# Kernel optimization log

Measured on AMD Instinct MI355X. Metric: run time of the kernel, lower is better.

## Reference

```python
import jax, jax.numpy as jnp
import numpy as np

D_MODEL = 768
NUM_HEADS = 12
D_K = D_MODEL // NUM_HEADS


def setup_inputs() -> dict:
    key = jax.random.key(0)
    ks = jax.random.split(key, 12)
    B, S = 4, 2048
    s = 1.0 / np.sqrt(D_MODEL)
    inp = {
        "query": jax.random.normal(ks[0], (B, S, D_MODEL), jnp.float32),
        "key": jax.random.normal(ks[1], (B, S, D_MODEL), jnp.float32),
        "value": jax.random.normal(ks[2], (B, S, D_MODEL), jnp.float32),
        "Wq": jax.random.normal(ks[3], (D_MODEL, D_MODEL), jnp.float32) * s,
        "bq": jnp.zeros((D_MODEL,), jnp.float32),
        "Wk": jax.random.normal(ks[4], (D_MODEL, D_MODEL), jnp.float32) * s,
        "bk": jnp.zeros((D_MODEL,), jnp.float32),
        "Wv": jax.random.normal(ks[5], (D_MODEL, D_MODEL), jnp.float32) * s,
        "bv": jnp.zeros((D_MODEL,), jnp.float32),
        "Wo": jax.random.normal(ks[6], (D_MODEL, D_MODEL), jnp.float32) * s,
        "bo": jnp.zeros((D_MODEL,), jnp.float32),
    }
    return inp


def _split_heads(x):
    B, S, _ = x.shape
    return x.reshape(B, S, NUM_HEADS, D_K).transpose(0, 2, 1, 3)  # [B,H,S,Dk]


def reference(query, key, value, Wq, bq, Wk, bk, Wv, bv, Wo, bo):
    # Linear projections (torch nn.Linear: x @ W.T + b)
    Q = _split_heads(query @ Wq.T + bq)
    K = _split_heads(key @ Wk.T + bk)
    V = _split_heads(value @ Wv.T + bv)
    scale = 1.0 / jnp.sqrt(jnp.asarray(D_K, Q.dtype))
    scores = jnp.einsum("bhqd,bhkd->bhqk", Q, K) * scale  # [B,H,S,S]
    attn = jax.nn.softmax(scores, axis=-1)
    # dropout is identity in eval mode
    out = jnp.einsum("bhqk,bhkd->bhqd", attn, V)  # [B,H,S,Dk]
    B, H, S, Dk = out.shape
    out = out.transpose(0, 2, 1, 3).reshape(B, S, H * Dk)
    return out @ Wo.T + bo
```

## Files before the change

### kernel.cpp

```cpp
#include <hip/hip_runtime.h>
#include <hip/hip_bf16.h>

typedef _Float16 half8 __attribute__((ext_vector_type(8)));
typedef _Float16 h4 __attribute__((ext_vector_type(4)));
typedef __fp16 fp16x2 __attribute__((ext_vector_type(2)));
typedef float f32x4 __attribute__((ext_vector_type(4)));

#define D_MODEL 768
#define NUM_HEADS 12
#define D_K 64
#define SEQ 2048
#define BATCH 4
#define M_TOTAL (BATCH * SEQ)
#define W_ELEMS (D_MODEL * D_MODEL)
#define X_ELEMS (M_TOTAL * D_MODEL)
#define QSCALE 0.18033688011112042f
#define SOFF 4.0f

__device__ __forceinline__ void gll16(const _Float16* g, _Float16* l) {
    __builtin_amdgcn_global_load_lds(
        (const __attribute__((address_space(1))) unsigned int*)g,
        (__attribute__((address_space(3))) unsigned int*)l,
        16, 0, 0);
}

__device__ __forceinline__ void pk2(float a, float b, _Float16* out) {
    fp16x2 r = __builtin_amdgcn_cvt_pkrtz(a, b);
    out[0] = (_Float16)r[0];
    out[1] = (_Float16)r[1];
}

__global__ void convert_all(
    const float* __restrict__ w0, const float* __restrict__ w1,
    const float* __restrict__ w2, const float* __restrict__ w3,
    const float* __restrict__ x0, const float* __restrict__ x1,
    const float* __restrict__ x2, _Float16* __restrict__ dst)
{
    const size_t W4 = W_ELEMS / 4, X4 = X_ELEMS / 4;
    size_t i = (size_t)blockIdx.x * blockDim.x + threadIdx.x;
    const float* src;
    size_t off;
    if (i < 4 * W4) {
        size_t slab = i / W4;
        off = i - slab * W4;
        src = (slab == 0) ? w0 : (slab == 1) ? w1 : (slab == 2) ? w2 : w3;
    } else {
        size_t j = i - 4 * W4;
        size_t slab = j / X4;
        off = j - slab * X4;
        src = (slab == 0) ? x0 : (slab == 1) ? x1 : x2;
    }
    float4 f = ((const float4*)src)[off];
    h4 h;
    h[0] = (_Float16)f.x; h[1] = (_Float16)f.y;
    h[2] = (_Float16)f.z; h[3] = (_Float16)f.w;
    ((h4*)dst)[i] = h;
}

__global__ __launch_bounds__(256) void gemm_qkv(
    const _Float16* __restrict__ Xall, const _Float16* __restrict__ Wall,
    const float* __restrict__ bq, const float* __restrict__ bk, const float* __restrict__ bv,
    _Float16* __restrict__ Qo, _Float16* __restrict__ Ko, _Float16* __restrict__ Vto)
{
    __shared__ __align__(16) char smem[36864];
    _Float16* As = (_Float16*)smem;
    _Float16* Bs = As + 128 * 64;

    const int z = blockIdx.z;
    const _Float16* X = Xall + (size_t)z * X_ELEMS;
    const _Float16* W = Wall + (size_t)z * W_ELEMS;

    const int t = threadIdx.x;
    const int w = t >> 6;
    const int l = t & 63;
    const int ln = t & 15;
    const int quad = (t >> 4) & 3;
    const int wm = w >> 1, wn = w & 1;
    const int m0 = blockIdx.x * 128, n0 = blockIdx.y * 128;

    const int srow = l >> 3;
    const int scol = (l & 7) ^ srow;

    f32x4 acc[4][4] = {};

    for (int k0 = 0; k0 < D_MODEL; k0 += 64) {
#pragma unroll
        for (int jj = 0; jj < 4; ++jj) {
            int j = w * 4 + jj;
            int row = j * 8 + srow;
            gll16(X + (size_t)(m0 + row) * D_MODEL + k0 + scol * 8, As + j * 512);
            gll16(W + (size_t)(n0 + row) * D_MODEL + k0 + scol * 8, Bs + j * 512);
        }
        __syncthreads();

#pragma unroll
        for (int kk = 0; kk < 2; ++kk) {
            half8 a[4], b[4];
#pragma unroll
            for (int i = 0; i < 4; ++i) {
                int ra = wm * 64 + i * 16 + ln;
                int rb = wn * 64 + i * 16 + ln;
                a[i] = *(const half8*)&As[ra * 64 + (((kk * 4 + quad) ^ (ln & 7)) * 8)];
                b[i] = *(const half8*)&Bs[rb * 64 + (((kk * 4 + quad) ^ (ln & 7)) * 8)];
            }
#pragma unroll
            for (int i = 0; i < 4; ++i)
#pragma unroll
                for (int j2 = 0; j2 < 4; ++j2)
                    acc[i][j2] = __builtin_amdgcn_mfma_f32_16x16x32_f16(a[i], b[j2], acc[i][j2], 0, 0, 0);
        }
        __syncthreads();
    }

    const float* bias = (z == 0) ? bq : (z == 1) ? bk : bv;
    if (z <= 1) {
        _Float16* dst = (z == 0) ? Qo : Ko;
#pragma unroll
        for (int i = 0; i < 4; ++i) {
#pragma unroll
            for (int j = 0; j < 4; ++j) {
                int n = n0 + wn * 64 + j * 16 + ln;
                int h = n >> 6, d = n & 63;
                float bn = bias[n];
#pragma unroll
                for (int r = 0; r < 4; ++r) {
                    int m = m0 + wm * 64 + i * 16 + quad * 4 + r;
                    int b_ = m >> 11, s_ = m & 2047;
                    float v = acc[i][j][r] + bn;
                    if (z == 0) v *= QSCALE;
                    dst[((size_t)((b_ * NUM_HEADS + h) * SEQ + s_)) * D_K + d] = (_Float16)v;
                }
            }
        }
    } else {
        _Float16* T = (_Float16*)smem + (size_t)w * (64 * 72);
#pragma unroll
        for (int i = 0; i < 4; ++i) {
#pragma unroll
            for (int j = 0; j < 4; ++j) {
                float bn = bias[n0 + wn * 64 + j * 16 + ln];
                h4 hh;
#pragma unroll
                for (int r = 0; r < 4; ++r) hh[r] = (_Float16)(acc[i][j][r] + bn);
                *(h4*)&T[(j * 16 + ln) * 72 + i * 16 + quad * 4] = hh;
            }
        }
        const int b_ = m0 >> 11;
        const int s0 = (m0 & 2047) + wm * 64;
        const int head = (n0 >> 6) + wn;
        _Float16* base = Vto + (size_t)(b_ * NUM_HEADS + head) * D_K * SEQ + s0;
#pragma unroll
        for (int r8 = 0; r8 < 8; ++r8) {
            int nl = r8 * 8 + (l >> 3);
            half8 v = *(const half8*)&T[nl * 72 + (l & 7) * 8];
            *(half8*)(base + (size_t)nl * SEQ + (l & 7) * 8) = v;
        }
    }
}

__global__ __launch_bounds__(256) void attn(
    const _Float16* __restrict__ Qg, const _Float16* __restrict__ Kg,
    const _Float16* __restrict__ Vtg, _Float16* __restrict__ ctx)
{
    __shared__ __align__(16) _Float16 Ks[2][64 * 64];
    __shared__ __align__(16) _Float16 Vs[2][64 * 64];

    const int t = threadIdx.x;
    const int w = t >> 6;
    const int l = t & 63;
    const int ln = t & 15;
    const int quad = (t >> 4) & 3;
    const int bh = blockIdx.y;
    const int q0 = blockIdx.x * 128 + w * 32;

    const _Float16* Qh = Qg + (size_t)bh * SEQ * D_K;
    const _Float16* Kh = Kg + (size_t)bh * SEQ * D_K;
    const _Float16* Vh = Vtg + (size_t)bh * D_K * SEQ;

    const int srow = l >> 3;
    const int scol = (l & 7) ^ srow;
    const int j0 = w * 2, j1 = w * 2 + 1;
    const _Float16* Ksrc0 = Kh + (size_t)(j0 * 8 + srow) * D_K + scol * 8;
    const _Float16* Ksrc1 = Kh + (size_t)(j1 * 8 + srow) * D_K + scol * 8;
    const _Float16* Vsrc0 = Vh + (size_t)(j0 * 8 + srow) * SEQ + scol * 8;
    const _Float16* Vsrc1 = Vh + (size_t)(j1 * 8 + srow) * SEQ + scol * 8;

    half8 qf[2][2];
#pragma unroll
    for (int qt = 0; qt < 2; ++qt)
#pragma unroll
        for (int dh = 0; dh < 2; ++dh)
            qf[qt][dh] = *(const half8*)(Qh + (size_t)(q0 + qt * 16 + ln) * D_K + dh * 32 + quad * 8);

    f32x4 acc[2][4] = {};
    f32x4 lsum[2] = {};

    gll16(Ksrc0, &Ks[0][j0 * 512]);
    gll16(Ksrc1, &Ks[0][j1 * 512]);
    gll16(Vsrc0, &Vs[0][j0 * 512]);
    gll16(Vsrc1, &Vs[0][j1 * 512]);
    __syncthreads();

    for (int c = 0; c < SEQ / 64; ++c) {
        const int cur = c & 1;
        if (c + 1 < SEQ / 64) {
            const size_t koff = (size_t)(c + 1) * 64 * D_K;
            const size_t voff = (size_t)(c + 1) * 64;
            gll16(Ksrc0 + koff, &Ks[cur ^ 1][j0 * 512]);
            gll16(Ksrc1 + koff, &Ks[cur ^ 1][j1 * 512]);
            gll16(Vsrc0 + voff, &Vs[cur ^ 1][j0 * 512]);
            gll16(Vsrc1 + voff, &Vs[cur ^ 1][j1 * 512]);
        }
        const _Float16* KsC = Ks[cur];
        const _Float16* VsC = Vs[cur];

        h4 pB[2][4];
#pragma unroll
        for (int kt = 0; kt < 4; ++kt) {
            half8 kf0 = *(const half8*)&KsC[(kt * 16 + ln) * 64 + ((quad ^ (ln & 7)) * 8)];
            half8 kf1 = *(const half8*)&KsC[(kt * 16 + ln) * 64 + (((4 + quad) ^ (ln & 7)) * 8)];
#pragma unroll
            for (int qt = 0; qt < 2; ++qt) {
                f32x4 s = {-SOFF, -SOFF, -SOFF, -SOFF};
                s = __builtin_amdgcn_mfma_f32_16x16x32_f16(kf0, qf[qt][0], s, 0, 0, 0);
                s = __builtin_amdgcn_mfma_f32_16x16x32_f16(kf1, qf[qt][1], s, 0, 0, 0);
                f32x4 p;
                p[0] = exp2f(s[0]); p[1] = exp2f(s[1]);
                p[2] = exp2f(s[2]); p[3] = exp2f(s[3]);
                lsum[qt] += p;
                h4 h;
                pk2(p[0], p[1], (_Float16*)&h);
                pk2(p[2], p[3], ((_Float16*)&h) + 2);
                pB[qt][kt] = h;
            }
        }

#pragma unroll
        for (int dt = 0; dt < 4; ++dt) {
#pragma unroll
            for (int kt = 0; kt < 4; ++kt) {
                int g = kt * 2 + (quad >> 1);
                h4 vf = *(const h4*)&VsC[(dt * 16 + ln) * 64 + ((g ^ (ln & 7)) * 8) + (quad & 1) * 4];
                acc[0][dt] = __builtin_amdgcn_mfma_f32_16x16x16f16(vf, pB[0][kt], acc[0][dt], 0, 0, 0);
                acc[1][dt] = __builtin_amdgcn_mfma_f32_16x16x16f16(vf, pB[1][kt], acc[1][dt], 0, 0, 0);
            }
        }
        __syncthreads();
    }

    const int h = bh % NUM_HEADS, b = bh / NUM_HEADS;
#pragma unroll
    for (int qt = 0; qt < 2; ++qt) {
        float lp = lsum[qt][0] + lsum[qt][1] + lsum[qt][2] + lsum[qt][3];
        lp += __shfl_xor(lp, 16);
        lp += __shfl_xor(lp, 32);
        float rinv = 1.0f / lp;
        int q = q0 + qt * 16 + ln;
#pragma unroll
        for (int dt = 0; dt < 4; ++dt) {
            h4 o;
            o[0] = (_Float16)(acc[qt][dt][0] * rinv);
            o[1] = (_Float16)(acc[qt][dt][1] * rinv);
            o[2] = (_Float16)(acc[qt][dt][2] * rinv);
            o[3] = (_Float16)(acc[qt][dt][3] * rinv);
            *(h4*)&ctx[((size_t)(b * SEQ + q)) * D_MODEL + h * D_K + dt * 16 + quad * 4] = o;
        }
    }
}

__global__ __launch_bounds__(256) void gemm_out(
    const _Float16* __restrict__ A, const _Float16* __restrict__ W,
    const float* __restrict__ bo, float* __restrict__ out)
{
    __shared__ __align__(16) _Float16 As[128 * 64];
    __shared__ __align__(16) _Float16 Bs[128 * 64];

    const int t = threadIdx.x;
    const int w = t >> 6;
    const int l = t & 63;
    const int ln = t & 15;
    const int quad = (t >> 4) & 3;
    const int wm = w >> 1, wn = w & 1;
    const int m0 = blockIdx.x * 128, n0 = blockIdx.y * 128;

    const int srow = l >> 3;
    const int scol = (l & 7) ^ srow;

    f32x4 acc[4][4] = {};

    for (int k0 = 0; k0 < D_MODEL; k0 += 64) {
#pragma unroll
        for (int jj = 0; jj < 4; ++jj) {
            int j = w * 4 + jj;
            int row = j * 8 + srow;
            gll16(A + (size_t)(m0 + row) * D_MODEL + k0 + scol * 8, As + j * 512);
            gll16(W + (size_t)(n0 + row) * D_MODEL + k0 + scol * 8, Bs + j * 512);
        }
        __syncthreads();

#pragma unroll
        for (int kk = 0; kk < 2; ++kk) {
            half8 a[4], b[4];
#pragma unroll
            for (int i = 0; i < 4; ++i) {
                int ra = wm * 64 + i * 16 + ln;
                int rb = wn * 64 + i * 16 + ln;
                a[i] = *(const half8*)&As[ra * 64 + (((kk * 4 + quad) ^ (ln & 7)) * 8)];
                b[i] = *(const half8*)&Bs[rb * 64 + (((kk * 4 + quad) ^ (ln & 7)) * 8)];
            }
#pragma unroll
            for (int i = 0; i < 4; ++i)
#pragma unroll
                for (int j2 = 0; j2 < 4; ++j2)
                    acc[i][j2] = __builtin_amdgcn_mfma_f32_16x16x32_f16(a[i], b[j2], acc[i][j2], 0, 0, 0);
        }
        __syncthreads();
    }

#pragma unroll
    for (int i = 0; i < 4; ++i) {
#pragma unroll
        for (int j = 0; j < 4; ++j) {
            int n = n0 + wn * 64 + j * 16 + ln;
            float bn = bo[n];
#pragma unroll
            for (int r = 0; r < 4; ++r) {
                int m = m0 + wm * 64 + i * 16 + quad * 4 + r;
                out[(size_t)m * D_MODEL + n] = acc[i][j][r] + bn;
            }
        }
    }
}

extern "C" void kernel_launch(void* const* d_in, const int* in_sizes, int n_in,
                              void* d_out, int out_size, void* d_ws, size_t ws_size,
                              hipStream_t stream) {
    const float* query = (const float*)d_in[0];
    const float* key   = (const float*)d_in[1];
    const float* value = (const float*)d_in[2];
    const float* Wq = (const float*)d_in[3];
    const float* bq = (const float*)d_in[4];
    const float* Wk = (const float*)d_in[5];
    const float* bk = (const float*)d_in[6];
    const float* Wv = (const float*)d_in[7];
    const float* bv = (const float*)d_in[8];
    const float* Wo = (const float*)d_in[9];
    const float* bo = (const float*)d_in[10];
    float* out = (float*)d_out;

    _Float16* ws = (_Float16*)d_ws;
    _Float16* Wb  = ws;
    _Float16* Xb  = Wb + 4 * (size_t)W_ELEMS;
    _Float16* Qb  = Xb + 3 * (size_t)X_ELEMS;
    _Float16* Kb  = Qb + (size_t)X_ELEMS;
    _Float16* Vtb = Kb + (size_t)X_ELEMS;
    _Float16* ctx = Vtb + (size_t)X_ELEMS;

    const size_t total4 = (4 * (size_t)W_ELEMS + 3 * (size_t)X_ELEMS) / 4;
    convert_all<<<(int)(total4 / 256), 256, 0, stream>>>(
        Wq, Wk, Wv, Wo, query, key, value, Wb);

    gemm_qkv<<<dim3(M_TOTAL / 128, D_MODEL / 128, 3), 256, 0, stream>>>(
        Xb, Wb, bq, bk, bv, Qb, Kb, Vtb);

    attn<<<dim3(SEQ / 128, BATCH * NUM_HEADS), 256, 0, stream>>>(Qb, Kb, Vtb, ctx);

    gemm_out<<<dim3(M_TOTAL / 128, D_MODEL / 128), 256, 0, stream>>>(
        ctx, Wb + 3 * (size_t)W_ELEMS, bo, out);
}
```

Measured before the change: 299.8 us.

## Single-buffer attention K/V tiles, preload V fragments, use fast exp2/rcp intrinsics

Replaces the double-buffered K/V shared-memory pipeline with a single buffer that is loaded and synchronized at the top of each chunk. It also preloads all V fragments into registers before the score computation, and switches exp2f and the final division to raw hardware intrinsics. Halving LDS use may allow more blocks per CU, and the intrinsics drop the range-handling code around exp2 and rcp. In exchange, global-to-LDS loads are no longer overlapped with compute, and the held V fragments raise register pressure.

```diff
diff --git a/kernel.cpp b/kernel.cpp
--- a/kernel.cpp
+++ b/kernel.cpp
@@ -162,8 +162,8 @@
     const _Float16* __restrict__ Qg, const _Float16* __restrict__ Kg,
     const _Float16* __restrict__ Vtg, _Float16* __restrict__ ctx)
 {
-    __shared__ __align__(16) _Float16 Ks[2][64 * 64];
-    __shared__ __align__(16) _Float16 Vs[2][64 * 64];
+    __shared__ __align__(16) _Float16 Ks[64 * 64];
+    __shared__ __align__(16) _Float16 Vs[64 * 64];
 
     const int t = threadIdx.x;
     const int w = t >> 6;
@@ -195,38 +195,39 @@
     f32x4 acc[2][4] = {};
     f32x4 lsum[2] = {};
 
-    gll16(Ksrc0, &Ks[0][j0 * 512]);
-    gll16(Ksrc1, &Ks[0][j1 * 512]);
-    gll16(Vsrc0, &Vs[0][j0 * 512]);
-    gll16(Vsrc1, &Vs[0][j1 * 512]);
-    __syncthreads();
-
     for (int c = 0; c < SEQ / 64; ++c) {
-        const int cur = c & 1;
-        if (c + 1 < SEQ / 64) {
-            const size_t koff = (size_t)(c + 1) * 64 * D_K;
-            const size_t voff = (size_t)(c + 1) * 64;
-            gll16(Ksrc0 + koff, &Ks[cur ^ 1][j0 * 512]);
-            gll16(Ksrc1 + koff, &Ks[cur ^ 1][j1 * 512]);
-            gll16(Vsrc0 + voff, &Vs[cur ^ 1][j0 * 512]);
-            gll16(Vsrc1 + voff, &Vs[cur ^ 1][j1 * 512]);
-        }
-        const _Float16* KsC = Ks[cur];
-        const _Float16* VsC = Vs[cur];
+        const size_t koff = (size_t)c * 64 * D_K;
+        const size_t voff = (size_t)c * 64;
+        gll16(Ksrc0 + koff, &Ks[j0 * 512]);
+        gll16(Ksrc1 + koff, &Ks[j1 * 512]);
+        gll16(Vsrc0 + voff, &Vs[j0 * 512]);
+        gll16(Vsrc1 + voff, &Vs[j1 * 512]);
+        __syncthreads();
+
+        h4 vfr[4][4];
+#pragma unroll
+        for (int dt = 0; dt < 4; ++dt)
+#pragma unroll
+            for (int kt = 0; kt < 4; ++kt) {
+                int g = kt * 2 + (quad >> 1);
+                vfr[dt][kt] = *(const h4*)&Vs[(dt * 16 + ln) * 64 + ((g ^ (ln & 7)) * 8) + (quad & 1) * 4];
+            }
 
         h4 pB[2][4];
 #pragma unroll
         for (int kt = 0; kt < 4; ++kt) {
-            half8 kf0 = *(const half8*)&KsC[(kt * 16 + ln) * 64 + ((quad ^ (ln & 7)) * 8)];
-            half8 kf1 = *(const half8*)&KsC[(kt * 16 + ln) * 64 + (((4 + quad) ^ (ln & 7)) * 8)];
+            half8 kf0 = *(const half8*)&Ks[(kt * 16 + ln) * 64 + ((quad ^ (ln & 7)) * 8)];
+            half8 kf1 = *(const half8*)&Ks[(kt * 16 + ln) * 64 + (((4 + quad) ^ (ln & 7)) * 8)];
 #pragma unroll
             for (int qt = 0; qt < 2; ++qt) {
                 f32x4 s = {-SOFF, -SOFF, -SOFF, -SOFF};
                 s = __builtin_amdgcn_mfma_f32_16x16x32_f16(kf0, qf[qt][0], s, 0, 0, 0);
                 s = __builtin_amdgcn_mfma_f32_16x16x32_f16(kf1, qf[qt][1], s, 0, 0, 0);
                 f32x4 p;
-                p[0] = exp2f(s[0]); p[1] = exp2f(s[1]);
-                p[2] = exp2f(s[2]); p[3] = exp2f(s[3]);
+                p[0] = __builtin_amdgcn_exp2f(s[0]);
+                p[1] = __builtin_amdgcn_exp2f(s[1]);
+                p[2] = __builtin_amdgcn_exp2f(s[2]);
+                p[3] = __builtin_amdgcn_exp2f(s[3]);
                 lsum[qt] += p;
                 h4 h;
                 pk2(p[0], p[1], (_Float16*)&h);
@@ -236,15 +237,12 @@
         }
 
 #pragma unroll
-        for (int dt = 0; dt < 4; ++dt) {
+        for (int dt = 0; dt < 4; ++dt)
 #pragma unroll
             for (int kt = 0; kt < 4; ++kt) {
-                int g = kt * 2 + (quad >> 1);
-                h4 vf = *(const h4*)&VsC[(dt * 16 + ln) * 64 + ((g ^ (ln & 7)) * 8) + (quad & 1) * 4];
-                acc[0][dt] = __builtin_amdgcn_mfma_f32_16x16x16f16(vf, pB[0][kt], acc[0][dt], 0, 0, 0);
-                acc[1][dt] = __builtin_amdgcn_mfma_f32_16x16x16f16(vf, pB[1][kt], acc[1][dt], 0, 0, 0);
-            }
-        }
+                acc[0][dt] = __builtin_amdgcn_mfma_f32_16x16x16f16(vfr[dt][kt], pB[0][kt], acc[0][dt], 0, 0, 0);
+                acc[1][dt] = __builtin_amdgcn_mfma_f32_16x16x16f16(vfr[dt][kt], pB[1][kt], acc[1][dt], 0, 0, 0);
+            }
         __syncthreads();
     }
 
@@ -254,7 +252,7 @@
         float lp = lsum[qt][0] + lsum[qt][1] + lsum[qt][2] + lsum[qt][3];
         lp += __shfl_xor(lp, 16);
         lp += __shfl_xor(lp, 32);
-        float rinv = 1.0f / lp;
+        float rinv = __builtin_amdgcn_rcpf(lp);
         int q = q0 + qt * 16 + ln;
 #pragma unroll
         for (int dt = 0; dt < 4; ++dt) {
```

Measured after the change: 271.4 us. -9.5%, faster.
